# Optimization experiments

Measured on AMD Instinct MI355X. Metric: run time of the kernel, lower is better.

## Reference

```python
import jax, jax.numpy as jnp
import numpy as np

B, T, D = 4, 1024, 1024
H, HD = 16, 64
DFF = 4096
EPS = 1e-5


def _ln(x, g, b):
    mu = jnp.mean(x, axis=-1, keepdims=True)
    var = jnp.var(x, axis=-1, keepdims=True)
    return (x - mu) * jax.lax.rsqrt(var + EPS) * g + b


def _attn(q_in, kv_in, wq, bq, wk, bk, wv, bv, wo, bo):
    # q_in: [B,Tq,D], kv_in: [B,Tk,D]
    Tq, Tk = q_in.shape[1], kv_in.shape[1]
    q = (q_in @ wq + bq).reshape(B, Tq, H, HD).transpose(0, 2, 1, 3)
    k = (kv_in @ wk + bk).reshape(B, Tk, H, HD).transpose(0, 2, 1, 3)
    v = (kv_in @ wv + bv).reshape(B, Tk, H, HD).transpose(0, 2, 1, 3)
    att = jnp.einsum('bhqd,bhkd->bhqk', q, k) * (1.0 / np.sqrt(HD))
    causal = jnp.tril(jnp.ones((Tq, Tk), dtype=bool))
    att = jnp.where(causal, att, -jnp.inf)
    att = jax.nn.softmax(att, axis=-1)
    y = jnp.einsum('bhqk,bhkd->bhqd', att, v)
    y = y.transpose(0, 2, 1, 3).reshape(B, Tq, H * HD)
    return y @ wo + bo


def setup_inputs() -> dict:
    key = jax.random.key(0)
    ks = jax.random.split(key, 20)
    g = lambda k, shp, scale: (jax.random.normal(k, shp, jnp.float32) * scale)
    s_d = 1.0 / np.sqrt(D)
    s_f = 1.0 / np.sqrt(DFF)
    inp = {
        'x_encoder': jax.random.normal(ks[0], (B, T, D), jnp.float32),
        'x': jax.random.normal(ks[1], (B, T, D), jnp.float32),
        'ln1_g': jnp.ones((D,), jnp.float32), 'ln1_b': jnp.zeros((D,), jnp.float32),
        'ln2_g': jnp.ones((D,), jnp.float32), 'ln2_b': jnp.zeros((D,), jnp.float32),
        'sa_wq': g(ks[2], (D, D), s_d), 'sa_bq': jnp.zeros((D,), jnp.float32),
        'sa_wk': g(ks[3], (D, D), s_d), 'sa_bk': jnp.zeros((D,), jnp.float32),
        'sa_wv': g(ks[4], (D, D), s_d), 'sa_bv': jnp.zeros((D,), jnp.float32),
        'sa_wo': g(ks[5], (D, D), s_d), 'sa_bo': jnp.zeros((D,), jnp.float32),
        'ca_wq': g(ks[6], (D, D), s_d), 'ca_bq': jnp.zeros((D,), jnp.float32),
        'ca_wk': g(ks[7], (D, D), s_d), 'ca_bk': jnp.zeros((D,), jnp.float32),
        'ca_wv': g(ks[8], (D, D), s_d), 'ca_bv': jnp.zeros((D,), jnp.float32),
        'ca_wo': g(ks[9], (D, D), s_d), 'ca_bo': jnp.zeros((D,), jnp.float32),
        'mlp_w1': g(ks[10], (D, DFF), s_d), 'mlp_b1': jnp.zeros((DFF,), jnp.float32),
        'mlp_w2': g(ks[11], (DFF, D), s_f), 'mlp_b2': jnp.zeros((D,), jnp.float32),
    }
    return inp


def reference(x_encoder, x, ln1_g, ln1_b, ln2_g, ln2_b,
              sa_wq, sa_bq, sa_wk, sa_bk, sa_wv, sa_bv, sa_wo, sa_bo,
              ca_wq, ca_bq, ca_wk, ca_bk, ca_wv, ca_bv, ca_wo, ca_bo,
              mlp_w1, mlp_b1, mlp_w2, mlp_b2):
    # x = x + SelfAttn(ln1(x))
    x = x + _attn(_ln(x, ln1_g, ln1_b), _ln(x, ln1_g, ln1_b),
                  sa_wq, sa_bq, sa_wk, sa_bk, sa_wv, sa_bv, sa_wo, sa_bo)
    # x = x + CrossAttn(x_encoder, ln1(x))  (note: ln1 reused, causal mask on dec x enc)
    x = x + _attn(_ln(x, ln1_g, ln1_b), x_encoder,
                  ca_wq, ca_bq, ca_wk, ca_bk, ca_wv, ca_bv, ca_wo, ca_bo)
    # MLP with exact GELU (torch nn.GELU default)
    h = _ln(x, ln2_g, ln2_b)
    h = jax.nn.gelu(h @ mlp_w1 + mlp_b1, approximate=False) @ mlp_w2 + mlp_b2
    return x + h
```

## Files before the change

kernel.cpp:

```cpp
#include <hip/hip_runtime.h>
#include <hip/hip_bf16.h>

typedef __bf16 bf16;
typedef __attribute__((ext_vector_type(8))) __bf16 bf16x8;
typedef __attribute__((ext_vector_type(4))) float f32x4;

#define MFMA16(a, b, c) __builtin_amdgcn_mfma_f32_16x16x32_bf16(a, b, c, 0, 0, 0)

#define LGKM_FENCE()                                      \
  do {                                                    \
    asm volatile("s_waitcnt lgkmcnt(0)" ::: "memory");    \
    __builtin_amdgcn_sched_barrier(0);                    \
  } while (0)

#define SCHED0() __builtin_amdgcn_sched_barrier(0)
#define SBAR() __builtin_amdgcn_s_barrier()
#define PRIO(x) __builtin_amdgcn_s_setprio(x)

typedef __attribute__((address_space(1))) void gvoid;
typedef __attribute__((address_space(3))) void lvoid;
__device__ __forceinline__ void gl16(const bf16* g, bf16* l) {
  __builtin_amdgcn_global_load_lds((gvoid*)g, (lvoid*)l, 16, 0, 0);
}


struct WPtrs { const float* p[8]; };

__global__ __launch_bounds__(256) void wtrans8_k(WPtrs wp, bf16* __restrict__ dst) {
  const float* w = wp.p[blockIdx.z];
  bf16* wt = dst + (size_t)blockIdx.z * 1024 * 1024;
  __shared__ float t[32][33];
  const int tx = threadIdx.x & 31, ty = threadIdx.x >> 5;
  const int nb = blockIdx.x * 32, kb = blockIdx.y * 32;
  for (int i = 0; i < 4; ++i)
    t[ty + i * 8][tx] = w[(size_t)(kb + ty + i * 8) * 1024 + nb + tx];
  __syncthreads();
  for (int i = 0; i < 4; ++i)
    wt[(size_t)(nb + ty + i * 8) * 1024 + kb + tx] = (bf16)t[tx][ty + i * 8];
}

__global__ __launch_bounds__(256) void wtrans_k(const float* __restrict__ w,
                                                bf16* __restrict__ wt,
                                                int K, int N) {
  __shared__ float t[32][33];
  const int tx = threadIdx.x & 31, ty = threadIdx.x >> 5;
  const int nb = blockIdx.x * 32, kb = blockIdx.y * 32;
  for (int i = 0; i < 4; ++i)
    t[ty + i * 8][tx] = w[(size_t)(kb + ty + i * 8) * N + nb + tx];
  __syncthreads();
  for (int i = 0; i < 4; ++i)
    wt[(size_t)(nb + ty + i * 8) * K + kb + tx] = (bf16)t[tx][ty + i * 8];
}

__global__ __launch_bounds__(256) void tobf_k(const float* __restrict__ in,
                                              bf16* __restrict__ out) {
  const int i = blockIdx.x * 256 + threadIdx.x;
  const float4 v = ((const float4*)in)[i];
  bf16* o = out + (size_t)i * 4;
  o[0] = (bf16)v.x; o[1] = (bf16)v.y; o[2] = (bf16)v.z; o[3] = (bf16)v.w;
}

struct B5 { const float* s[5]; };
__global__ __launch_bounds__(256) void bpack_k(B5 bp, float* __restrict__ bq3,
                                               float* __restrict__ bkv2) {
  const int i = blockIdx.x;
  float* d = (i < 3) ? bq3 + i * 1024 : bkv2 + (i - 3) * 1024;
  ((float4*)d)[threadIdx.x] = ((const float4*)bp.s[i])[threadIdx.x];
}

__global__ __launch_bounds__(512) void vtrans_k(const bf16* __restrict__ Vp,
                                                bf16* __restrict__ Vt) {
  __shared__ bf16 tl[64][72];
  const int tt = blockIdx.x, bh = blockIdx.y;
  const int b = bh >> 4, h = bh & 15;
  const int tid = threadIdx.x;
  const int row = tid >> 3, ck = tid & 7;
  *(bf16x8*)&tl[row][ck * 8] =
      *(const bf16x8*)&Vp[(size_t)(b * 1024 + tt * 64 + row) * 1024 + h * 64 + ck * 8];
  __syncthreads();
  const int hd = tid >> 3, tc = tid & 7;
  bf16 tmp[8];
#pragma unroll
  for (int e = 0; e < 8; ++e) tmp[e] = tl[tc * 8 + e][hd];
  *(bf16x8*)&Vt[(size_t)(bh * 64 + hd) * 1024 + tt * 64 + tc * 8] = *(bf16x8*)tmp;
}

__global__ __launch_bounds__(256) void ln_k(const float* __restrict__ x,
                                            const float* __restrict__ g,
                                            const float* __restrict__ bta,
                                            bf16* __restrict__ out) {
  const int row = blockIdx.x, tid = threadIdx.x;
  const float4 v = ((const float4*)(x + (size_t)row * 1024))[tid];
  float s = v.x + v.y + v.z + v.w;
  float sq = v.x * v.x + v.y * v.y + v.z * v.z + v.w * v.w;
  for (int d = 1; d < 64; d <<= 1) { s += __shfl_xor(s, d); sq += __shfl_xor(sq, d); }
  __shared__ float rs[4], rq[4];
  const int w = tid >> 6, lane = tid & 63;
  if (lane == 0) { rs[w] = s; rq[w] = sq; }
  __syncthreads();
  s = rs[0] + rs[1] + rs[2] + rs[3];
  sq = rq[0] + rq[1] + rq[2] + rq[3];
  const float mean = s * (1.0f / 1024.0f);
  const float var = sq * (1.0f / 1024.0f) - mean * mean;
  const float rstd = rsqrtf(var + 1e-5f);
  const float4 gv = ((const float4*)g)[tid];
  const float4 bv = ((const float4*)bta)[tid];
  bf16* o = out + (size_t)row * 1024 + tid * 4;
  o[0] = (bf16)((v.x - mean) * rstd * gv.x + bv.x);
  o[1] = (bf16)((v.y - mean) * rstd * gv.y + bv.y);
  o[2] = (bf16)((v.z - mean) * rstd * gv.z + bv.z);
  o[3] = (bf16)((v.w - mean) * rstd * gv.w + bv.w);
}

template <int EPI>
__global__ __launch_bounds__(256) void gemm_k(const bf16* __restrict__ A,
                                              const bf16* __restrict__ Bt,
                                              const float* __restrict__ bias,
                                              const float* __restrict__ res,
                                              void* __restrict__ o0,
                                              void* __restrict__ o1,
                                              void* __restrict__ o2,
                                              int K, int N) {
  __shared__ bf16 As[2][128 * 64];
  __shared__ bf16 Bs[2][128 * 64];
  const int tid = threadIdx.x;
  const int lane = tid & 63, w = tid >> 6;
  const int wr = w >> 1, wc = w & 1;
  const int l15 = lane & 15, l4 = lane >> 4;
  const int gx = gridDim.x;
  const int nwg = gx * gridDim.y;
  const int flat = blockIdx.x + blockIdx.y * gx;
  const int swz = (flat & 7) * (nwg >> 3) + (flat >> 3);
  const size_t bm = swz / gx, bn = swz % gx;
  const bf16* Ab = A + bm * 128 * (size_t)K;
  const bf16* Bb = Bt + bn * 128 * (size_t)K;

  const f32x4 zero4 = {0.f, 0.f, 0.f, 0.f};
  f32x4 acc[4][4];
  for (int m = 0; m < 4; ++m)
    for (int n = 0; n < 4; ++n) acc[m][n] = zero4;

  const int srow = lane >> 3;
  const int gck = ((lane & 7) ^ srow) * 8;
  auto stage = [&](int buf, int t) {
    const int kt = t * 64;
    for (int j = 0; j < 4; ++j) {
      const int row = w * 32 + j * 8 + srow;
      bf16* la = As[buf] + (w * 256 + j * 64 + lane) * 8;
      bf16* lb = Bs[buf] + (w * 256 + j * 64 + lane) * 8;
      gl16(Ab + (size_t)row * K + kt + gck, la);
      gl16(Bb + (size_t)row * K + kt + gck, lb);
    }
  };
  const int xr = l15 & 7;
  const int c0 = (l4 ^ xr) * 8, c1 = ((4 + l4) ^ xr) * 8;
  auto compute = [&](int buf) {
    bf16x8 af[4][2], bfr[4][2];
    for (int m = 0; m < 4; ++m) {
      const int ro = (wr * 64 + m * 16 + l15) * 64;
      af[m][0] = *(const bf16x8*)&As[buf][ro + c0];
      af[m][1] = *(const bf16x8*)&As[buf][ro + c1];
    }
    for (int n = 0; n < 4; ++n) {
      const int ro = (wc * 64 + n * 16 + l15) * 64;
      bfr[n][0] = *(const bf16x8*)&Bs[buf][ro + c0];
      bfr[n][1] = *(const bf16x8*)&Bs[buf][ro + c1];
    }
    PRIO(1);
    for (int m = 0; m < 4; ++m)
      for (int n = 0; n < 4; ++n) {
        acc[m][n] = MFMA16(af[m][0], bfr[n][0], acc[m][n]);
        acc[m][n] = MFMA16(af[m][1], bfr[n][1], acc[m][n]);
      }
    PRIO(0);
  };

  const int nt = K >> 6;
  stage(0, 0);
  stage(1, 1);
  int cur = 0;
  for (int t = 0; t < nt - 2; ++t) {
    asm volatile("s_waitcnt vmcnt(8)" ::: "memory");
    SBAR(); SCHED0();
    compute(cur);
    SCHED0(); SBAR(); SCHED0();
    stage(cur, t + 2);
    cur ^= 1;
  }
  asm volatile("s_waitcnt vmcnt(8)" ::: "memory");
  SBAR(); SCHED0();
  compute(cur);
  cur ^= 1;
  asm volatile("s_waitcnt vmcnt(0)" ::: "memory");
  SBAR(); SCHED0();
  compute(cur);

  for (int m = 0; m < 4; ++m) {
    const int row0 = (int)bm * 128 + wr * 64 + m * 16 + l4 * 4;
    for (int n = 0; n < 4; ++n) {
      const int col = (int)bn * 128 + wc * 64 + n * 16 + l15;
      const float bv = bias[col];
      for (int r = 0; r < 4; ++r) {
        const int row = row0 + r;
        const float v = acc[m][n][r] + bv;
        if constexpr (EPI == 0) {
          ((bf16*)o0)[(size_t)row * N + col] = (bf16)v;
        } else if constexpr (EPI == 2) {
          ((float*)o0)[(size_t)row * N + col] = v + res[(size_t)row * N + col];
        } else if constexpr (EPI == 3) {
          const float gl = 0.5f * v * (1.0f + erff(v * 0.70710678118f));
          ((bf16*)o0)[(size_t)row * N + col] = (bf16)gl;
        } else {
          const int which = col >> 10, c = col & 1023;
          bf16* op = (bf16*)(which == 0 ? o0 : (which == 1 ? o1 : o2));
          op[(size_t)row * 1024 + c] = (bf16)v;
        }
      }
    }
  }
}

template <int EPI>
__global__ __launch_bounds__(256) void gemm64_k(const bf16* __restrict__ A,
                                                const bf16* __restrict__ Bt,
                                                const float* __restrict__ bias,
                                                const float* __restrict__ res,
                                                void* __restrict__ o0,
                                                int K, int N) {
  __shared__ bf16 As[2][128 * 64];
  __shared__ bf16 Bs[2][64 * 64];
  const int tid = threadIdx.x;
  const int lane = tid & 63, w = tid >> 6;
  const int l15 = lane & 15, l4 = lane >> 4;
  const int gx = gridDim.x;
  const int nwg = gx * gridDim.y;
  const int flat = blockIdx.x + blockIdx.y * gx;
  const int swz = (flat & 7) * (nwg >> 3) + (flat >> 3);
  const size_t bm = swz / gx, bn = swz % gx;
  const bf16* Ab = A + bm * 128 * (size_t)K;
  const bf16* Bb = Bt + bn * 64 * (size_t)K;

  const f32x4 zero4 = {0.f, 0.f, 0.f, 0.f};
  f32x4 acc[2][4];
  for (int m = 0; m < 2; ++m)
    for (int n = 0; n < 4; ++n) acc[m][n] = zero4;

  const int srow = lane >> 3;
  const int gck = ((lane & 7) ^ srow) * 8;
  auto stage = [&](int buf, int t) {
    const int kt = t * 64;
    for (int j = 0; j < 4; ++j) {
      const int row = w * 32 + j * 8 + srow;
      gl16(Ab + (size_t)row * K + kt + gck, As[buf] + (w * 256 + j * 64 + lane) * 8);
    }
    for (int j = 0; j < 2; ++j) {
      const int row = w * 16 + j * 8 + srow;
      gl16(Bb + (size_t)row * K + kt + gck, Bs[buf] + (w * 128 + j * 64 + lane) * 8);
    }
  };
  const int xr = l15 & 7;
  const int c0 = (l4 ^ xr) * 8, c1 = ((4 + l4) ^ xr) * 8;
  auto compute = [&](int buf) {
    bf16x8 af[2][2], bfr[4][2];
    for (int m = 0; m < 2; ++m) {
      const int ro = (w * 32 + m * 16 + l15) * 64;
      af[m][0] = *(const bf16x8*)&As[buf][ro + c0];
      af[m][1] = *(const bf16x8*)&As[buf][ro + c1];
    }
    for (int n = 0; n < 4; ++n) {
      const int ro = (n * 16 + l15) * 64;
      bfr[n][0] = *(const bf16x8*)&Bs[buf][ro + c0];
      bfr[n][1] = *(const bf16x8*)&Bs[buf][ro + c1];
    }
    PRIO(1);
    for (int m = 0; m < 2; ++m)
      for (int n = 0; n < 4; ++n) {
        acc[m][n] = MFMA16(af[m][0], bfr[n][0], acc[m][n]);
        acc[m][n] = MFMA16(af[m][1], bfr[n][1], acc[m][n]);
      }
    PRIO(0);
  };

  const int nt = K >> 6;
  stage(0, 0);
  stage(1, 1);
  int cur = 0;
  for (int t = 0; t < nt - 2; ++t) {
    asm volatile("s_waitcnt vmcnt(6)" ::: "memory");
    SBAR(); SCHED0();
    compute(cur);
    SCHED0(); SBAR(); SCHED0();
    stage(cur, t + 2);
    cur ^= 1;
  }
  asm volatile("s_waitcnt vmcnt(6)" ::: "memory");
  SBAR(); SCHED0();
  compute(cur);
  cur ^= 1;
  asm volatile("s_waitcnt vmcnt(0)" ::: "memory");
  SBAR(); SCHED0();
  compute(cur);

  for (int m = 0; m < 2; ++m) {
    const int row0 = (int)bm * 128 + w * 32 + m * 16 + l4 * 4;
    for (int n = 0; n < 4; ++n) {
      const int col = (int)bn * 64 + n * 16 + l15;
      const float bv = bias[col];
      for (int r = 0; r < 4; ++r) {
        const int row = row0 + r;
        const float v = acc[m][n][r] + bv;
        if constexpr (EPI == 0) {
          ((bf16*)o0)[(size_t)row * N + col] = (bf16)v;
        } else {
          ((float*)o0)[(size_t)row * N + col] = v + res[(size_t)row * N + col];
        }
      }
    }
  }
}

__global__ __launch_bounds__(512) void attn_k(const bf16* __restrict__ Q,
                                              const bf16* __restrict__ Kb,
                                              const bf16* __restrict__ Vt,
                                              bf16* __restrict__ O) {
  __shared__ bf16 Ks[2][64 * 64];
  __shared__ bf16 Vs[2][64 * 64];
  __shared__ bf16 Plds[8][16][72];
  const int bx = blockIdx.x, bh = blockIdx.y;
  const int b = bh >> 4, h = bh & 15;
  const int tid = threadIdx.x, lane = tid & 63, w = tid >> 6;
  const int myqt = (w < 4) ? bx : (15 - bx);
  const int qbase = myqt * 64 + (w & 3) * 16;
  const int l15 = lane & 15, l4 = lane >> 4;
  const int nt = 16 - bx;

  const bf16* Qp = Q + (size_t)(b * 1024 + qbase + l15) * 1024 + h * 64 + l4 * 8;
  bf16x8 qf0 = *(const bf16x8*)Qp;
  bf16x8 qf1 = *(const bf16x8*)(Qp + 32);
  for (int i = 0; i < 8; ++i) {
    qf0[i] = (bf16)((float)qf0[i] * 0.125f);
    qf1[i] = (bf16)((float)qf1[i] * 0.125f);
  }
  bf16x8 onesf;
  for (int i = 0; i < 8; ++i) onesf[i] = (bf16)1.0f;

  const f32x4 zero4 = {0.f, 0.f, 0.f, 0.f};
  f32x4 o[4], ol;
  float mrow[4];
  for (int d = 0; d < 4; ++d) o[d] = zero4;
  ol = zero4;
  for (int r = 0; r < 4; ++r) mrow[r] = -1e30f;

  const int qrow0 = qbase + l4 * 4;

  const int srow = tid >> 3;
  const int cg = (tid & 7) ^ (srow & 7);
  const bf16* Kg = Kb + (size_t)(b * 1024 + srow) * 1024 + h * 64 + cg * 8;
  const bf16* Vg = Vt + (size_t)(bh * 64 + srow) * 1024 + cg * 8;
  auto stage = [&](int buf, int t) {
    gl16(Kg + (size_t)t * 64 * 1024, Ks[buf] + tid * 8);
    gl16(Vg + t * 64, Vs[buf] + tid * 8);
  };

  const int xr = l15 & 7;
  const int fc0 = (l4 ^ xr) * 8, fc1 = ((4 + l4) ^ xr) * 8;

  auto compute = [&](int buf, int kt) {
    const int kbase = kt * 64;
    f32x4 s[4];
    for (int n = 0; n < 4; ++n) s[n] = zero4;
    PRIO(1);
    for (int n = 0; n < 4; ++n) {
      const int ro = (n * 16 + l15) * 64;
      const bf16x8 kf0 = *(const bf16x8*)&Ks[buf][ro + fc0];
      const bf16x8 kf1 = *(const bf16x8*)&Ks[buf][ro + fc1];
      s[n] = MFMA16(qf0, kf0, s[n]);
      s[n] = MFMA16(qf1, kf1, s[n]);
    }
    PRIO(0);
    if (kt == myqt) {
      for (int n = 0; n < 4; ++n) {
        const int kc = kbase + n * 16 + l15;
        for (int r = 0; r < 4; ++r)
          if (kc > qrow0 + r) s[n][r] = -1e30f;
      }
    }
    float mx[4];
    for (int r = 0; r < 4; ++r)
      mx[r] = fmaxf(fmaxf(s[0][r], s[1][r]), fmaxf(s[2][r], s[3][r]));
    for (int d0 = 1; d0 < 16; d0 <<= 1)
      for (int r = 0; r < 4; ++r) mx[r] = fmaxf(mx[r], __shfl_xor(mx[r], d0));
    float alpha[4];
    for (int r = 0; r < 4; ++r) {
      const float mnew = fmaxf(mrow[r], mx[r]);
      alpha[r] = __expf(mrow[r] - mnew);
      mrow[r] = mnew;
    }
    for (int n = 0; n < 4; ++n)
      for (int r = 0; r < 4; ++r) s[n][r] = __expf(s[n][r] - mrow[r]);
    for (int d = 0; d < 4; ++d)
      for (int r = 0; r < 4; ++r) o[d][r] *= alpha[r];
    for (int r = 0; r < 4; ++r) ol[r] *= alpha[r];

    LGKM_FENCE();
    for (int r = 0; r < 4; ++r)
      for (int n = 0; n < 4; ++n)
        Plds[w][l4 * 4 + r][n * 16 + l15] = (bf16)s[n][r];
    LGKM_FENCE();
    const bf16x8 pf0 = *(const bf16x8*)&Plds[w][l15][l4 * 8];
    const bf16x8 pf1 = *(const bf16x8*)&Plds[w][l15][32 + l4 * 8];

    PRIO(1);
    for (int d = 0; d < 4; ++d) {
      const int ro = (d * 16 + l15) * 64;
      const bf16x8 vf0 = *(const bf16x8*)&Vs[buf][ro + fc0];
      const bf16x8 vf1 = *(const bf16x8*)&Vs[buf][ro + fc1];
      o[d] = MFMA16(pf0, vf0, o[d]);
      o[d] = MFMA16(pf1, vf1, o[d]);
    }
    ol = MFMA16(pf0, onesf, ol);
    ol = MFMA16(pf1, onesf, ol);
    PRIO(0);
  };

  stage(0, 0);
  stage(1, 1);
  int cur = 0;
  for (int t = 0; t < nt - 2; ++t) {
    asm volatile("s_waitcnt vmcnt(2)" ::: "memory");
    SBAR(); SCHED0();
    if (t <= myqt) compute(cur, t);
    SCHED0(); SBAR(); SCHED0();
    stage(cur, t + 2);
    cur ^= 1;
  }
  asm volatile("s_waitcnt vmcnt(2)" ::: "memory");
  SBAR(); SCHED0();
  if (nt - 2 <= myqt) compute(cur, nt - 2);
  cur ^= 1;
  asm volatile("s_waitcnt vmcnt(0)" ::: "memory");
  SBAR(); SCHED0();
  if (nt - 1 <= myqt) compute(cur, nt - 1);

  for (int r = 0; r < 4; ++r) {
    const float inv = 1.0f / ol[r];
    for (int d = 0; d < 4; ++d) {
      O[(size_t)(b * 1024 + qbase + l4 * 4 + r) * 1024 + h * 64 + d * 16 + l15] =
          (bf16)(o[d][r] * inv);
    }
  }
}

extern "C" void kernel_launch(void* const* d_in, const int* in_sizes, int n_in,
                              void* d_out, int out_size, void* d_ws, size_t ws_size,
                              hipStream_t stream) {
  const float* x_enc = (const float*)d_in[0];
  const float* x     = (const float*)d_in[1];
  const float* ln1_g = (const float*)d_in[2];
  const float* ln1_b = (const float*)d_in[3];
  const float* ln2_g = (const float*)d_in[4];
  const float* ln2_b = (const float*)d_in[5];
  const float* sa_wq = (const float*)d_in[6];  const float* sa_bq = (const float*)d_in[7];
  const float* sa_wk = (const float*)d_in[8];  const float* sa_bk = (const float*)d_in[9];
  const float* sa_wv = (const float*)d_in[10]; const float* sa_bv = (const float*)d_in[11];
  const float* sa_wo = (const float*)d_in[12]; const float* sa_bo = (const float*)d_in[13];
  const float* ca_wq = (const float*)d_in[14]; const float* ca_bq = (const float*)d_in[15];
  const float* ca_wk = (const float*)d_in[16]; const float* ca_bk = (const float*)d_in[17];
  const float* ca_wv = (const float*)d_in[18]; const float* ca_bv = (const float*)d_in[19];
  const float* ca_wo = (const float*)d_in[20]; const float* ca_bo = (const float*)d_in[21];
  const float* mlp_w1 = (const float*)d_in[22]; const float* mlp_b1 = (const float*)d_in[23];
  const float* mlp_w2 = (const float*)d_in[24]; const float* mlp_b2 = (const float*)d_in[25];

  char* ws = (char*)d_ws;
  size_t off = 0;
  auto take = [&](size_t bytes) { char* p = ws + off; off += (bytes + 255) & ~(size_t)255; return p; };

  bf16* wt8 = (bf16*)take((size_t)8 * 1024 * 1024 * 2);
  bf16* w1t   = (bf16*)take((size_t)4096 * 1024 * 2);
  bf16* w2t   = (bf16*)take((size_t)1024 * 4096 * 2);
  bf16* lnbuf = (bf16*)take((size_t)4096 * 1024 * 2);
  bf16* xe_bf = (bf16*)take((size_t)4096 * 1024 * 2);
  bf16* Qb    = (bf16*)take((size_t)4096 * 1024 * 2);
  bf16* Kbf   = (bf16*)take((size_t)4096 * 1024 * 2);
  bf16* Vpb   = (bf16*)take((size_t)4096 * 1024 * 2);
  bf16* Vtb   = (bf16*)take((size_t)4096 * 1024 * 2);
  bf16* AOb   = (bf16*)take((size_t)4096 * 1024 * 2);
  float* x1   = (float*)take((size_t)4096 * 1024 * 4);
  float* x2   = (float*)take((size_t)4096 * 1024 * 4);
  bf16* Hb    = (bf16*)take((size_t)4096 * 4096 * 2);
  float* bq3  = (float*)take((size_t)3072 * 4);
  float* bkv2 = (float*)take((size_t)2048 * 4);

  bf16* wt[8];
  for (int i = 0; i < 8; ++i) wt[i] = wt8 + (size_t)i * 1024 * 1024;

  const dim3 blk(256);
  WPtrs wp = {{sa_wq, sa_wk, sa_wv, sa_wo, ca_wq, ca_wk, ca_wv, ca_wo}};
  wtrans8_k<<<dim3(32, 32, 8), blk, 0, stream>>>(wp, wt8);
  wtrans_k<<<dim3(128, 32), blk, 0, stream>>>(mlp_w1, w1t, 1024, 4096);
  wtrans_k<<<dim3(32, 128), blk, 0, stream>>>(mlp_w2, w2t, 4096, 1024);
  tobf_k<<<4096, blk, 0, stream>>>(x_enc, xe_bf);
  B5 bp = {{sa_bq, sa_bk, sa_bv, ca_bk, ca_bv}};
  bpack_k<<<5, blk, 0, stream>>>(bp, bq3, bkv2);

  ln_k<<<4096, blk, 0, stream>>>(x, ln1_g, ln1_b, lnbuf);
  gemm_k<4><<<dim3(24, 32), blk, 0, stream>>>(lnbuf, wt[0], bq3, nullptr,
                                              Qb, Kbf, Vpb, 1024, 3072);
  vtrans_k<<<dim3(16, 64), dim3(512), 0, stream>>>(Vpb, Vtb);
  attn_k<<<dim3(8, 64), dim3(512), 0, stream>>>(Qb, Kbf, Vtb, AOb);
  gemm64_k<2><<<dim3(16, 32), blk, 0, stream>>>(AOb, wt[3], sa_bo, x, x1, 1024, 1024);

  ln_k<<<4096, blk, 0, stream>>>(x1, ln1_g, ln1_b, lnbuf);
  gemm64_k<0><<<dim3(16, 32), blk, 0, stream>>>(lnbuf, wt[4], ca_bq, nullptr, Qb, 1024, 1024);
  gemm_k<5><<<dim3(16, 32), blk, 0, stream>>>(xe_bf, wt[5], bkv2, nullptr,
                                              Kbf, Vpb, nullptr, 1024, 2048);
  vtrans_k<<<dim3(16, 64), dim3(512), 0, stream>>>(Vpb, Vtb);
  attn_k<<<dim3(8, 64), dim3(512), 0, stream>>>(Qb, Kbf, Vtb, AOb);
  gemm64_k<2><<<dim3(16, 32), blk, 0, stream>>>(AOb, wt[7], ca_bo, x1, x2, 1024, 1024);

  ln_k<<<4096, blk, 0, stream>>>(x2, ln2_g, ln2_b, lnbuf);
  gemm_k<3><<<dim3(32, 32), blk, 0, stream>>>(lnbuf, w1t, mlp_b1, nullptr,
                                              Hb, nullptr, nullptr, 1024, 4096);
  gemm64_k<2><<<dim3(16, 32), blk, 0, stream>>>(Hb, w2t, mlp_b2, x2,
                                                (float*)d_out, 4096, 1024);

  (void)in_sizes; (void)n_in; (void)out_size; (void)ws_size;
}
```

Measured before the change: 354.0 us.

## Halve GEMM K-tile to 32 with two-rows-per-LDS-line swizzled layout

Both GEMM kernels now stage K-tiles of 32 instead of 64. Each 64-element LDS line holds two 32-wide matrix rows, with a new XOR swizzle and matching fragment indexing, and the vmcnt waits are adjusted to the smaller per-stage load counts. This halves LDS use per block, which may raise occupancy. In exchange the loop runs twice as many iterations, each with half the MFMA work between barriers, so the extra synchronisation and shallower pipelining could hurt.

```diff
diff --git a/kernel.cpp b/kernel.cpp
--- a/kernel.cpp
+++ b/kernel.cpp
@@ -121,8 +121,8 @@
                                               void* __restrict__ o1,
                                               void* __restrict__ o2,
                                               int K, int N) {
-  __shared__ bf16 As[2][128 * 64];
-  __shared__ bf16 Bs[2][128 * 64];
+  __shared__ bf16 As[2][64 * 64];
+  __shared__ bf16 Bs[2][64 * 64];
   const int tid = threadIdx.x;
   const int lane = tid & 63, w = tid >> 6;
   const int wr = w >> 1, wc = w & 1;
@@ -140,54 +140,49 @@
   for (int m = 0; m < 4; ++m)
     for (int n = 0; n < 4; ++n) acc[m][n] = zero4;
 
-  const int srow = lane >> 3;
-  const int gck = ((lane & 7) ^ srow) * 8;
+  const int su = (lane & 7) ^ (lane >> 3);
+  const int grow = w * 16 + (lane >> 3) * 2 + (su >> 2);
+  const int gkc = (su & 3) * 8;
   auto stage = [&](int buf, int t) {
-    const int kt = t * 64;
-    for (int j = 0; j < 4; ++j) {
-      const int row = w * 32 + j * 8 + srow;
-      bf16* la = As[buf] + (w * 256 + j * 64 + lane) * 8;
-      bf16* lb = Bs[buf] + (w * 256 + j * 64 + lane) * 8;
-      gl16(Ab + (size_t)row * K + kt + gck, la);
-      gl16(Bb + (size_t)row * K + kt + gck, lb);
-    }
+    const int kt = t * 32;
+    bf16* la = As[buf] + (w * 64 + lane) * 8;
+    bf16* lb = Bs[buf] + (w * 64 + lane) * 8;
+    gl16(Ab + (size_t)grow * K + kt + gkc, la);
+    gl16(Ab + (size_t)(grow + 64) * K + kt + gkc, la + 2048);
+    gl16(Bb + (size_t)grow * K + kt + gkc, lb);
+    gl16(Bb + (size_t)(grow + 64) * K + kt + gkc, lb + 2048);
   };
-  const int xr = l15 & 7;
-  const int c0 = (l4 ^ xr) * 8, c1 = ((4 + l4) ^ xr) * 8;
+  const int rh = l15 >> 1, rb = (l15 & 1) << 2;
   auto compute = [&](int buf) {
-    bf16x8 af[4][2], bfr[4][2];
+    bf16x8 af[4], bfr[4];
     for (int m = 0; m < 4; ++m) {
-      const int ro = (wr * 64 + m * 16 + l15) * 64;
-      af[m][0] = *(const bf16x8*)&As[buf][ro + c0];
-      af[m][1] = *(const bf16x8*)&As[buf][ro + c1];
+      const int line = wr * 32 + m * 8 + rh;
+      af[m] = *(const bf16x8*)&As[buf][line * 64 + ((rb | l4) ^ (line & 7)) * 8];
     }
     for (int n = 0; n < 4; ++n) {
-      const int ro = (wc * 64 + n * 16 + l15) * 64;
-      bfr[n][0] = *(const bf16x8*)&Bs[buf][ro + c0];
-      bfr[n][1] = *(const bf16x8*)&Bs[buf][ro + c1];
+      const int line = wc * 32 + n * 8 + rh;
+      bfr[n] = *(const bf16x8*)&Bs[buf][line * 64 + ((rb | l4) ^ (line & 7)) * 8];
     }
     PRIO(1);
     for (int m = 0; m < 4; ++m)
-      for (int n = 0; n < 4; ++n) {
-        acc[m][n] = MFMA16(af[m][0], bfr[n][0], acc[m][n]);
-        acc[m][n] = MFMA16(af[m][1], bfr[n][1], acc[m][n]);
-      }
+      for (int n = 0; n < 4; ++n)
+        acc[m][n] = MFMA16(af[m], bfr[n], acc[m][n]);
     PRIO(0);
   };
 
-  const int nt = K >> 6;
+  const int nt = K >> 5;
   stage(0, 0);
   stage(1, 1);
   int cur = 0;
   for (int t = 0; t < nt - 2; ++t) {
-    asm volatile("s_waitcnt vmcnt(8)" ::: "memory");
+    asm volatile("s_waitcnt vmcnt(4)" ::: "memory");
     SBAR(); SCHED0();
     compute(cur);
     SCHED0(); SBAR(); SCHED0();
     stage(cur, t + 2);
     cur ^= 1;
   }
-  asm volatile("s_waitcnt vmcnt(8)" ::: "memory");
+  asm volatile("s_waitcnt vmcnt(4)" ::: "memory");
   SBAR(); SCHED0();
   compute(cur);
   cur ^= 1;
@@ -227,8 +222,8 @@
                                                 const float* __restrict__ res,
                                                 void* __restrict__ o0,
                                                 int K, int N) {
-  __shared__ bf16 As[2][128 * 64];
-  __shared__ bf16 Bs[2][64 * 64];
+  __shared__ bf16 As[2][64 * 64];
+  __shared__ bf16 Bs[2][32 * 64];
   const int tid = threadIdx.x;
   const int lane = tid & 63, w = tid >> 6;
   const int l15 = lane & 15, l4 = lane >> 4;
@@ -245,55 +240,47 @@
   for (int m = 0; m < 2; ++m)
     for (int n = 0; n < 4; ++n) acc[m][n] = zero4;
 
-  const int srow = lane >> 3;
-  const int gck = ((lane & 7) ^ srow) * 8;
+  const int su = (lane & 7) ^ (lane >> 3);
+  const int grow = w * 16 + (lane >> 3) * 2 + (su >> 2);
+  const int gkc = (su & 3) * 8;
   auto stage = [&](int buf, int t) {
-    const int kt = t * 64;
-    for (int j = 0; j < 4; ++j) {
-      const int row = w * 32 + j * 8 + srow;
-      gl16(Ab + (size_t)row * K + kt + gck, As[buf] + (w * 256 + j * 64 + lane) * 8);
-    }
-    for (int j = 0; j < 2; ++j) {
-      const int row = w * 16 + j * 8 + srow;
-      gl16(Bb + (size_t)row * K + kt + gck, Bs[buf] + (w * 128 + j * 64 + lane) * 8);
-    }
+    const int kt = t * 32;
+    bf16* la = As[buf] + (w * 64 + lane) * 8;
+    gl16(Ab + (size_t)grow * K + kt + gkc, la);
+    gl16(Ab + (size_t)(grow + 64) * K + kt + gkc, la + 2048);
+    gl16(Bb + (size_t)grow * K + kt + gkc, Bs[buf] + (w * 64 + lane) * 8);
   };
-  const int xr = l15 & 7;
-  const int c0 = (l4 ^ xr) * 8, c1 = ((4 + l4) ^ xr) * 8;
+  const int rh = l15 >> 1, rb = (l15 & 1) << 2;
   auto compute = [&](int buf) {
-    bf16x8 af[2][2], bfr[4][2];
+    bf16x8 af[2], bfr[4];
     for (int m = 0; m < 2; ++m) {
-      const int ro = (w * 32 + m * 16 + l15) * 64;
-      af[m][0] = *(const bf16x8*)&As[buf][ro + c0];
-      af[m][1] = *(const bf16x8*)&As[buf][ro + c1];
+      const int line = w * 16 + m * 8 + rh;
+      af[m] = *(const bf16x8*)&As[buf][line * 64 + ((rb | l4) ^ (line & 7)) * 8];
     }
     for (int n = 0; n < 4; ++n) {
-      const int ro = (n * 16 + l15) * 64;
-      bfr[n][0] = *(const bf16x8*)&Bs[buf][ro + c0];
-      bfr[n][1] = *(const bf16x8*)&Bs[buf][ro + c1];
+      const int line = n * 8 + rh;
+      bfr[n] = *(const bf16x8*)&Bs[buf][line * 64 + ((rb | l4) ^ (line & 7)) * 8];
     }
     PRIO(1);
     for (int m = 0; m < 2; ++m)
-      for (int n = 0; n < 4; ++n) {
-        acc[m][n] = MFMA16(af[m][0], bfr[n][0], acc[m][n]);
-        acc[m][n] = MFMA16(af[m][1], bfr[n][1], acc[m][n]);
-      }
+      for (int n = 0; n < 4; ++n)
+        acc[m][n] = MFMA16(af[m], bfr[n], acc[m][n]);
     PRIO(0);
   };
 
-  const int nt = K >> 6;
+  const int nt = K >> 5;
   stage(0, 0);
   stage(1, 1);
   int cur = 0;
   for (int t = 0; t < nt - 2; ++t) {
-    asm volatile("s_waitcnt vmcnt(6)" ::: "memory");
+    asm volatile("s_waitcnt vmcnt(3)" ::: "memory");
     SBAR(); SCHED0();
     compute(cur);
     SCHED0(); SBAR(); SCHED0();
     stage(cur, t + 2);
     cur ^= 1;
   }
-  asm volatile("s_waitcnt vmcnt(6)" ::: "memory");
+  asm volatile("s_waitcnt vmcnt(3)" ::: "memory");
   SBAR(); SCHED0();
   compute(cur);
   cur ^= 1;
```

Result: slower. 384.9 us (+8.7%).

## Merge self-attn QKV and cross-attn KV GEMMs, batch V transposes, bf16 residuals

Applied to the files above, without the earlier changes.

Fuses the self-attention QKV projection and the cross-attention KV projection into a single GEMM launch over a 40x32 tile grid. Both V transposes are done in one launch using the z dimension. The intermediate residual streams x1 and x2 are stored in bf16 instead of fp32, with LayerNorm and the GEMM epilogues templated to read bf16. The aim is to cut launch count, fill the GPU better on the smaller KV GEMM, and reduce residual memory traffic, at the cost of lower residual precision.

```diff
diff --git a/kernel.cpp b/kernel.cpp
--- a/kernel.cpp
+++ b/kernel.cpp
@@ -2,6 +2,7 @@
 #include <hip/hip_bf16.h>
 
 typedef __bf16 bf16;
+typedef __attribute__((ext_vector_type(4))) __bf16 bf16x4;
 typedef __attribute__((ext_vector_type(8))) __bf16 bf16x8;
 typedef __attribute__((ext_vector_type(4))) float f32x4;
 
@@ -68,8 +69,12 @@
   ((float4*)d)[threadIdx.x] = ((const float4*)bp.s[i])[threadIdx.x];
 }
 
-__global__ __launch_bounds__(512) void vtrans_k(const bf16* __restrict__ Vp,
-                                                bf16* __restrict__ Vt) {
+__global__ __launch_bounds__(512) void vtrans_k(const bf16* __restrict__ V0,
+                                                const bf16* __restrict__ V1,
+                                                bf16* __restrict__ T0,
+                                                bf16* __restrict__ T1) {
+  const bf16* Vp = blockIdx.z ? V1 : V0;
+  bf16* Vt = blockIdx.z ? T1 : T0;
   __shared__ bf16 tl[64][72];
   const int tt = blockIdx.x, bh = blockIdx.y;
   const int b = bh >> 4, h = bh & 15;
@@ -85,14 +90,22 @@
   *(bf16x8*)&Vt[(size_t)(bh * 64 + hd) * 1024 + tt * 64 + tc * 8] = *(bf16x8*)tmp;
 }
 
-__global__ __launch_bounds__(256) void ln_k(const float* __restrict__ x,
+template <typename TIN>
+__global__ __launch_bounds__(256) void ln_k(const TIN* __restrict__ x,
                                             const float* __restrict__ g,
                                             const float* __restrict__ bta,
                                             bf16* __restrict__ out) {
   const int row = blockIdx.x, tid = threadIdx.x;
-  const float4 v = ((const float4*)(x + (size_t)row * 1024))[tid];
-  float s = v.x + v.y + v.z + v.w;
-  float sq = v.x * v.x + v.y * v.y + v.z * v.z + v.w * v.w;
+  float v0, v1, v2, v3;
+  if constexpr (sizeof(TIN) == 4) {
+    const float4 v = ((const float4*)((const float*)x + (size_t)row * 1024))[tid];
+    v0 = v.x; v1 = v.y; v2 = v.z; v3 = v.w;
+  } else {
+    const bf16x4 v = *(const bf16x4*)((const bf16*)x + (size_t)row * 1024 + tid * 4);
+    v0 = (float)v[0]; v1 = (float)v[1]; v2 = (float)v[2]; v3 = (float)v[3];
+  }
+  float s = v0 + v1 + v2 + v3;
+  float sq = v0 * v0 + v1 * v1 + v2 * v2 + v3 * v3;
   for (int d = 1; d < 64; d <<= 1) { s += __shfl_xor(s, d); sq += __shfl_xor(sq, d); }
   __shared__ float rs[4], rq[4];
   const int w = tid >> 6, lane = tid & 63;
@@ -106,20 +119,17 @@
   const float4 gv = ((const float4*)g)[tid];
   const float4 bv = ((const float4*)bta)[tid];
   bf16* o = out + (size_t)row * 1024 + tid * 4;
-  o[0] = (bf16)((v.x - mean) * rstd * gv.x + bv.x);
-  o[1] = (bf16)((v.y - mean) * rstd * gv.y + bv.y);
-  o[2] = (bf16)((v.z - mean) * rstd * gv.z + bv.z);
-  o[3] = (bf16)((v.w - mean) * rstd * gv.w + bv.w);
+  o[0] = (bf16)((v0 - mean) * rstd * gv.x + bv.x);
+  o[1] = (bf16)((v1 - mean) * rstd * gv.y + bv.y);
+  o[2] = (bf16)((v2 - mean) * rstd * gv.z + bv.z);
+  o[3] = (bf16)((v3 - mean) * rstd * gv.w + bv.w);
 }
 
 template <int EPI>
 __global__ __launch_bounds__(256) void gemm_k(const bf16* __restrict__ A,
                                               const bf16* __restrict__ Bt,
                                               const float* __restrict__ bias,
-                                              const float* __restrict__ res,
                                               void* __restrict__ o0,
-                                              void* __restrict__ o1,
-                                              void* __restrict__ o2,
                                               int K, int N) {
   __shared__ bf16 As[2][128 * 64];
   __shared__ bf16 Bs[2][128 * 64];
@@ -203,18 +213,112 @@
       for (int r = 0; r < 4; ++r) {
         const int row = row0 + r;
         const float v = acc[m][n][r] + bv;
-        if constexpr (EPI == 0) {
-          ((bf16*)o0)[(size_t)row * N + col] = (bf16)v;
-        } else if constexpr (EPI == 2) {
-          ((float*)o0)[(size_t)row * N + col] = v + res[(size_t)row * N + col];
-        } else if constexpr (EPI == 3) {
-          const float gl = 0.5f * v * (1.0f + erff(v * 0.70710678118f));
-          ((bf16*)o0)[(size_t)row * N + col] = (bf16)gl;
-        } else {
-          const int which = col >> 10, c = col & 1023;
-          bf16* op = (bf16*)(which == 0 ? o0 : (which == 1 ? o1 : o2));
-          op[(size_t)row * 1024 + c] = (bf16)v;
-        }
+        const float gl = 0.5f * v * (1.0f + erff(v * 0.70710678118f));
+        ((bf16*)o0)[(size_t)row * N + col] = (bf16)gl;
+      }
+    }
+  }
+}
+
+__global__ __launch_bounds__(256) void gemmqkv_k(const bf16* __restrict__ Aln,
+                                                 const bf16* __restrict__ Axe,
+                                                 const bf16* __restrict__ wtq,
+                                                 const bf16* __restrict__ wtkv,
+                                                 const float* __restrict__ bq3,
+                                                 const float* __restrict__ bkv2,
+                                                 bf16* __restrict__ Qb,
+                                                 bf16* __restrict__ Kb1,
+                                                 bf16* __restrict__ Vp1,
+                                                 bf16* __restrict__ Kb2,
+                                                 bf16* __restrict__ Vp2) {
+  const int K = 1024;
+  __shared__ bf16 As[2][128 * 64];
+  __shared__ bf16 Bs[2][128 * 64];
+  const int tid = threadIdx.x;
+  const int lane = tid & 63, w = tid >> 6;
+  const int wr = w >> 1, wc = w & 1;
+  const int l15 = lane & 15, l4 = lane >> 4;
+  const int gx = 40;
+  const int nwg = 40 * 32;
+  const int flat = blockIdx.x + blockIdx.y * gx;
+  const int swz = (flat & 7) * (nwg >> 3) + (flat >> 3);
+  const size_t bm = swz / gx, bn = swz % gx;
+  const bool qkv = bn < 24;
+  const bf16* Ab = (qkv ? Aln : Axe) + bm * 128 * (size_t)K;
+  const bf16* Bb = qkv ? (wtq + bn * 128 * (size_t)K)
+                       : (wtkv + (bn - 24) * 128 * (size_t)K);
+
+  const f32x4 zero4 = {0.f, 0.f, 0.f, 0.f};
+  f32x4 acc[4][4];
+  for (int m = 0; m < 4; ++m)
+    for (int n = 0; n < 4; ++n) acc[m][n] = zero4;
+
+  const int srow = lane >> 3;
+  const int gck = ((lane & 7) ^ srow) * 8;
+  auto stage = [&](int buf, int t) {
+    const int kt = t * 64;
+    for (int j = 0; j < 4; ++j) {
+      const int row = w * 32 + j * 8 + srow;
+      bf16* la = As[buf] + (w * 256 + j * 64 + lane) * 8;
+      bf16* lb = Bs[buf] + (w * 256 + j * 64 + lane) * 8;
+      gl16(Ab + (size_t)row * K + kt + gck, la);
+      gl16(Bb + (size_t)row * K + kt + gck, lb);
+    }
+  };
+  const int xr = l15 & 7;
+  const int c0 = (l4 ^ xr) * 8, c1 = ((4 + l4) ^ xr) * 8;
+  auto compute = [&](int buf) {
+    bf16x8 af[4][2], bfr[4][2];
+    for (int m = 0; m < 4; ++m) {
+      const int ro = (wr * 64 + m * 16 + l15) * 64;
+      af[m][0] = *(const bf16x8*)&As[buf][ro + c0];
+      af[m][1] = *(const bf16x8*)&As[buf][ro + c1];
+    }
+    for (int n = 0; n < 4; ++n) {
+      const int ro = (wc * 64 + n * 16 + l15) * 64;
+      bfr[n][0] = *(const bf16x8*)&Bs[buf][ro + c0];
+      bfr[n][1] = *(const bf16x8*)&Bs[buf][ro + c1];
+    }
+    PRIO(1);
+    for (int m = 0; m < 4; ++m)
+      for (int n = 0; n < 4; ++n) {
+        acc[m][n] = MFMA16(af[m][0], bfr[n][0], acc[m][n]);
+        acc[m][n] = MFMA16(af[m][1], bfr[n][1], acc[m][n]);
+      }
+    PRIO(0);
+  };
+
+  const int nt = K >> 6;
+  stage(0, 0);
+  stage(1, 1);
+  int cur = 0;
+  for (int t = 0; t < nt - 2; ++t) {
+    asm volatile("s_waitcnt vmcnt(8)" ::: "memory");
+    SBAR(); SCHED0();
+    compute(cur);
+    SCHED0(); SBAR(); SCHED0();
+    stage(cur, t + 2);
+    cur ^= 1;
+  }
+  asm volatile("s_waitcnt vmcnt(8)" ::: "memory");
+  SBAR(); SCHED0();
+  compute(cur);
+  cur ^= 1;
+  asm volatile("s_waitcnt vmcnt(0)" ::: "memory");
+  SBAR(); SCHED0();
+  compute(cur);
+
+  for (int m = 0; m < 4; ++m) {
+    const int row0 = (int)bm * 128 + wr * 64 + m * 16 + l4 * 4;
+    for (int n = 0; n < 4; ++n) {
+      const int coln = (qkv ? (int)bn : (int)bn - 24) * 128 + wc * 64 + n * 16 + l15;
+      const float bv = qkv ? bq3[coln] : bkv2[coln];
+      const int which = coln >> 10, c = coln & 1023;
+      bf16* op = qkv ? (which == 0 ? Qb : (which == 1 ? Kb1 : Vp1))
+                     : (which == 0 ? Kb2 : Vp2);
+      for (int r = 0; r < 4; ++r) {
+        const int row = row0 + r;
+        op[(size_t)row * 1024 + c] = (bf16)(acc[m][n][r] + bv);
       }
     }
   }
@@ -224,7 +328,7 @@
 __global__ __launch_bounds__(256) void gemm64_k(const bf16* __restrict__ A,
                                                 const bf16* __restrict__ Bt,
                                                 const float* __restrict__ bias,
-                                                const float* __restrict__ res,
+                                                const void* __restrict__ res,
                                                 void* __restrict__ o0,
                                                 int K, int N) {
   __shared__ bf16 As[2][128 * 64];
@@ -308,11 +412,19 @@
       const float bv = bias[col];
       for (int r = 0; r < 4; ++r) {
         const int row = row0 + r;
-        const float v = acc[m][n][r] + bv;
+        const size_t idx = (size_t)row * N + col;
+        float v = acc[m][n][r] + bv;
         if constexpr (EPI == 0) {
-          ((bf16*)o0)[(size_t)row * N + col] = (bf16)v;
+          ((bf16*)o0)[idx] = (bf16)v;
+        } else if constexpr (EPI == 2) {
+          v += ((const float*)res)[idx];
+          ((bf16*)o0)[idx] = (bf16)v;
+        } else if constexpr (EPI == 4) {
+          v += (float)((const bf16*)res)[idx];
+          ((bf16*)o0)[idx] = (bf16)v;
         } else {
-          ((float*)o0)[(size_t)row * N + col] = v + res[(size_t)row * N + col];
+          v += (float)((const bf16*)res)[idx];
+          ((float*)o0)[idx] = v;
         }
       }
     }
@@ -481,12 +593,15 @@
   bf16* lnbuf = (bf16*)take((size_t)4096 * 1024 * 2);
   bf16* xe_bf = (bf16*)take((size_t)4096 * 1024 * 2);
   bf16* Qb    = (bf16*)take((size_t)4096 * 1024 * 2);
-  bf16* Kbf   = (bf16*)take((size_t)4096 * 1024 * 2);
-  bf16* Vpb   = (bf16*)take((size_t)4096 * 1024 * 2);
-  bf16* Vtb   = (bf16*)take((size_t)4096 * 1024 * 2);
+  bf16* Kb1   = (bf16*)take((size_t)4096 * 1024 * 2);
+  bf16* Vp1   = (bf16*)take((size_t)4096 * 1024 * 2);
+  bf16* Vt1   = (bf16*)take((size_t)4096 * 1024 * 2);
+  bf16* Kb2   = (bf16*)take((size_t)4096 * 1024 * 2);
+  bf16* Vp2   = (bf16*)take((size_t)4096 * 1024 * 2);
+  bf16* Vt2   = (bf16*)take((size_t)4096 * 1024 * 2);
   bf16* AOb   = (bf16*)take((size_t)4096 * 1024 * 2);
-  float* x1   = (float*)take((size_t)4096 * 1024 * 4);
-  float* x2   = (float*)take((size_t)4096 * 1024 * 4);
+  bf16* x1    = (bf16*)take((size_t)4096 * 1024 * 2);
+  bf16* x2    = (bf16*)take((size_t)4096 * 1024 * 2);
   bf16* Hb    = (bf16*)take((size_t)4096 * 4096 * 2);
   float* bq3  = (float*)take((size_t)3072 * 4);
   float* bkv2 = (float*)take((size_t)2048 * 4);
@@ -503,25 +618,22 @@
   B5 bp = {{sa_bq, sa_bk, sa_bv, ca_bk, ca_bv}};
   bpack_k<<<5, blk, 0, stream>>>(bp, bq3, bkv2);
 
-  ln_k<<<4096, blk, 0, stream>>>(x, ln1_g, ln1_b, lnbuf);
-  gemm_k<4><<<dim3(24, 32), blk, 0, stream>>>(lnbuf, wt[0], bq3, nullptr,
-                                              Qb, Kbf, Vpb, 1024, 3072);
-  vtrans_k<<<dim3(16, 64), dim3(512), 0, stream>>>(Vpb, Vtb);
-  attn_k<<<dim3(8, 64), dim3(512), 0, stream>>>(Qb, Kbf, Vtb, AOb);
+  ln_k<float><<<4096, blk, 0, stream>>>(x, ln1_g, ln1_b, lnbuf);
+  gemmqkv_k<<<dim3(40, 32), blk, 0, stream>>>(lnbuf, xe_bf, wt[0], wt[5],
+                                              bq3, bkv2, Qb, Kb1, Vp1, Kb2, Vp2);
+  vtrans_k<<<dim3(16, 64, 2), dim3(512), 0, stream>>>(Vp1, Vp2, Vt1, Vt2);
+
+  attn_k<<<dim3(8, 64), dim3(512), 0, stream>>>(Qb, Kb1, Vt1, AOb);
   gemm64_k<2><<<dim3(16, 32), blk, 0, stream>>>(AOb, wt[3], sa_bo, x, x1, 1024, 1024);
 
-  ln_k<<<4096, blk, 0, stream>>>(x1, ln1_g, ln1_b, lnbuf);
+  ln_k<bf16><<<4096, blk, 0, stream>>>(x1, ln1_g, ln1_b, lnbuf);
   gemm64_k<0><<<dim3(16, 32), blk, 0, stream>>>(lnbuf, wt[4], ca_bq, nullptr, Qb, 1024, 1024);
-  gemm_k<5><<<dim3(16, 32), blk, 0, stream>>>(xe_bf, wt[5], bkv2, nullptr,
-                                              Kbf, Vpb, nullptr, 1024, 2048);
-  vtrans_k<<<dim3(16, 64), dim3(512), 0, stream>>>(Vpb, Vtb);
-  attn_k<<<dim3(8, 64), dim3(512), 0, stream>>>(Qb, Kbf, Vtb, AOb);
-  gemm64_k<2><<<dim3(16, 32), blk, 0, stream>>>(AOb, wt[7], ca_bo, x1, x2, 1024, 1024);
-
-  ln_k<<<4096, blk, 0, stream>>>(x2, ln2_g, ln2_b, lnbuf);
-  gemm_k<3><<<dim3(32, 32), blk, 0, stream>>>(lnbuf, w1t, mlp_b1, nullptr,
-                                              Hb, nullptr, nullptr, 1024, 4096);
-  gemm64_k<2><<<dim3(16, 32), blk, 0, stream>>>(Hb, w2t, mlp_b2, x2,
+  attn_k<<<dim3(8, 64), dim3(512), 0, stream>>>(Qb, Kb2, Vt2, AOb);
+  gemm64_k<4><<<dim3(16, 32), blk, 0, stream>>>(AOb, wt[7], ca_bo, x1, x2, 1024, 1024);
+
+  ln_k<bf16><<<4096, blk, 0, stream>>>(x2, ln2_g, ln2_b, lnbuf);
+  gemm_k<3><<<dim3(32, 32), blk, 0, stream>>>(lnbuf, w1t, mlp_b1, Hb, 1024, 4096);
+  gemm64_k<5><<<dim3(16, 32), blk, 0, stream>>>(Hb, w2t, mlp_b2, x2,
                                                 (float*)d_out, 4096, 1024);
 
   (void)in_sizes; (void)n_in; (void)out_size; (void)ws_size;
```

Result: faster. 342.5 us (-3.2%).
